# Optimization experiments

Hardware: AMD Instinct MI355X
Metric: run time of the kernel (lower is better)

The kernel has to match this reference:

```python
import jax, jax.numpy as jnp
import numpy as np

B, A, S, D = 32, 32, 128, 1024
N, H = 16, 64


def setup_inputs() -> dict:
    key = jax.random.key(0)
    k1, k2, k3, k4, k5, k6 = jax.random.split(key, 6)
    encoder_outputs = jax.random.normal(k1, (B, A, S, D), dtype=jnp.float32)
    doc_attention_mask = jax.random.randint(k2, (B, A), 0, 2, dtype=jnp.int32)
    # DenseEinsum params: kernel [D, N, H], bias [N, H] (glorot / zeros)
    scale = (6.0 / (D + N * H)) ** 0.5
    wq = jax.random.uniform(k3, (D, N, H), jnp.float32, -scale, scale)
    wk = jax.random.uniform(k4, (D, N, H), jnp.float32, -scale, scale)
    bq = jnp.zeros((N, H), jnp.float32)
    bk = jnp.zeros((N, H), jnp.float32)
    return {"encoder_outputs": encoder_outputs, "doc_attention_mask": doc_attention_mask,
            "wq": wq, "bq": bq, "wk": wk, "bk": bk}


def reference(encoder_outputs, doc_attention_mask, wq, bq, wk, bk):
    # CLS embedding per doc: [B, A, D]
    cls = encoder_outputs[:, :, 0, :]
    m = doc_attention_mask.astype(jnp.float32)  # [B, A]
    # projections -> [B, A, N, H], masked per doc
    query = (jnp.einsum('bad,dnh->banh', cls, wq) + bq) * m[:, :, None, None]
    key = (jnp.einsum('bad,dnh->banh', cls, wk) + bk) * m[:, :, None, None]
    # pairwise doc scores [B, N, A, A]
    att = jnp.einsum('bxnh,bynh->bnxy', query, key)
    num_docs = att.shape[-1]
    diag_mask = 1.0 - jnp.eye(num_docs, dtype=att.dtype)  # zero diagonal
    att = att * diag_mask
    # BNXY -> BNX (sum over Y) -> BX (sum over N)
    logits = att.sum(axis=(1, 3))  # [B, A]
    infadder = (1.0 - m) * -100000.0
    return jax.nn.softmax(logits + infadder, axis=-1)
```

## Files before the change

### kernel.cpp

```cpp
#include <hip/hip_runtime.h>
#include <hip/hip_bf16.h>


#define RB 1024
#define DD 1024
#define CC 1024
#define ENC_ROW_STRIDE (128 * 1024)

#define BM 64
#define BN 64
#define BK 32

__global__ __launch_bounds__(256) void gemm_qk_logits(
    const float* __restrict__ enc, const int* __restrict__ mask,
    const float* __restrict__ wq, const float* __restrict__ wk,
    const float* __restrict__ bq, const float* __restrict__ bk,
    float* __restrict__ logits)
{
    __shared__ __align__(16) float As[BK][BM + 4];
    __shared__ __align__(16) float Bqs[BK][BN];
    __shared__ __align__(16) float Bks[BK][BN];
    __shared__ float ksum_s[2][BN];

    const int tid  = threadIdx.x;
    const int row0 = blockIdx.y * BM;
    const int col0 = blockIdx.x * BN;

    const int tx = tid & 15;
    const int ty = tid >> 4;

    const int ar = tid >> 5, ac = tid & 31;
    const int br = tid >> 6, bc = tid & 63;

    float accq[4][4] = {{0.f}}, acck[4][4] = {{0.f}};

    for (int k0 = 0; k0 < DD; k0 += BK) {
        #pragma unroll
        for (int r = 0; r < 8; ++r) {
            int m = ar + 8 * r;
            As[ac][m] = enc[(size_t)(row0 + m) * ENC_ROW_STRIDE + k0 + ac];
        }
        #pragma unroll
        for (int r = 0; r < 8; ++r) {
            int kk = br + 4 * r;
            size_t off = (size_t)(k0 + kk) * CC + col0 + bc;
            Bqs[kk][bc] = wq[off];
            Bks[kk][bc] = wk[off];
        }
        __syncthreads();

        #pragma unroll
        for (int kk = 0; kk < BK; ++kk) {
            float4 a4 = *(const float4*)&As[kk][ty * 4];
            float4 q4 = *(const float4*)&Bqs[kk][tx * 4];
            float4 k4 = *(const float4*)&Bks[kk][tx * 4];
            float a[4]   = {a4.x, a4.y, a4.z, a4.w};
            float bqv[4] = {q4.x, q4.y, q4.z, q4.w};
            float bkv[4] = {k4.x, k4.y, k4.z, k4.w};
            #pragma unroll
            for (int i = 0; i < 4; ++i) {
                #pragma unroll
                for (int j = 0; j < 4; ++j) {
                    accq[i][j] = fmaf(a[i], bqv[j], accq[i][j]);
                    acck[i][j] = fmaf(a[i], bkv[j], acck[i][j]);
                }
            }
        }
        __syncthreads();
    }

    const int bat = ty >> 3;

    if (tid < 2 * BN) ((float*)ksum_s)[tid] = 0.f;
    __syncthreads();

    float qv[4][4], kv[4][4];
    float mrow[4];
    #pragma unroll
    for (int i = 0; i < 4; ++i) {
        int row = row0 + ty * 4 + i;
        mrow[i] = (float)mask[row];
    }
    #pragma unroll
    for (int j = 0; j < 4; ++j) {
        int col = col0 + tx * 4 + j;
        float bqc = bq[col], bkc = bk[col];
        float ks = 0.f;
        #pragma unroll
        for (int i = 0; i < 4; ++i) {
            qv[i][j] = (accq[i][j] + bqc) * mrow[i];
            kv[i][j] = (acck[i][j] + bkc) * mrow[i];
            ks += kv[i][j];
        }
        atomicAdd(&ksum_s[bat][tx * 4 + j], ks);
    }
    __syncthreads();

    #pragma unroll
    for (int i = 0; i < 4; ++i) {
        float p = 0.f;
        #pragma unroll
        for (int j = 0; j < 4; ++j)
            p = fmaf(qv[i][j], ksum_s[bat][tx * 4 + j] - kv[i][j], p);
        #pragma unroll
        for (int off = 8; off; off >>= 1) p += __shfl_down(p, off, 16);
        if (tx == 0) atomicAdd(&logits[row0 + ty * 4 + i], p);
    }
}

__global__ __launch_bounds__(1024) void softmax32(
    const float* __restrict__ logits, const int* __restrict__ mask,
    float* __restrict__ out)
{
    const int t = threadIdx.x;
    float m = (float)mask[t];
    float v = logits[t] + (1.f - m) * -100000.f;
    float mx = v;
    #pragma unroll
    for (int off = 16; off; off >>= 1) mx = fmaxf(mx, __shfl_xor(mx, off, 32));
    float e = expf(v - mx);
    float s = e;
    #pragma unroll
    for (int off = 16; off; off >>= 1) s += __shfl_xor(s, off, 32);
    out[t] = e / s;
}

extern "C" void kernel_launch(void* const* d_in, const int* in_sizes, int n_in,
                              void* d_out, int out_size, void* d_ws, size_t ws_size,
                              hipStream_t stream) {
    const float* enc  = (const float*)d_in[0];
    const int*   mask = (const int*)  d_in[1];
    const float* wq   = (const float*)d_in[2];
    const float* bq   = (const float*)d_in[3];
    const float* wk   = (const float*)d_in[4];
    const float* bk   = (const float*)d_in[5];
    float* out = (float*)d_out;

    float* logits = (float*)d_ws;
    hipMemsetAsync(logits, 0, RB * sizeof(float), stream);

    gemm_qk_logits<<<dim3(CC / BN, RB / BM), 256, 0, stream>>>(
        enc, mask, wq, wk, bq, bk, logits);
    softmax32<<<1, 1024, 0, stream>>>(logits, mask, out);
}
```

Measured before the change: 698.8 us.

## Replace FP32 SIMT GEMM with bf16 MFMA GEMM using prepped transposed weights

Adds a prep kernel that converts the CLS rows and transposed Wq/Wk to bf16. The main GEMM now uses 16x16x32 bf16 MFMA instructions with direct global-to-LDS loads into XOR-swizzled shared tiles. Per-column-block partial logits are written to a buffer and summed in the softmax kernel, which replaces the memset and global atomics. This trades fp32 precision for bf16 inputs and adds an extra pass that rewrites the weights on every call.

```diff
diff --git a/kernel.cpp b/kernel.cpp
--- a/kernel.cpp
+++ b/kernel.cpp
@@ -1,5 +1,6 @@
 #include <hip/hip_runtime.h>
 #include <hip/hip_bf16.h>
+#include <stdint.h>
 
 
 #define RB 1024
@@ -7,114 +8,216 @@
 #define CC 1024
 #define ENC_ROW_STRIDE (128 * 1024)
 
-#define BM 64
-#define BN 64
-#define BK 32
-
-__global__ __launch_bounds__(256) void gemm_qk_logits(
-    const float* __restrict__ enc, const int* __restrict__ mask,
+typedef __attribute__((ext_vector_type(8))) short short8;
+typedef __attribute__((ext_vector_type(4))) float float4v;
+
+__device__ __forceinline__ unsigned short f2bf(float f) {
+    union { float f; unsigned int u; } x; x.f = f;
+    unsigned int r = (x.u + 0x7fffu + ((x.u >> 16) & 1u)) >> 16;
+    return (unsigned short)r;
+}
+
+__device__ __forceinline__ void gld_lds16(const void* g, void* l) {
+    __builtin_amdgcn_global_load_lds(
+        (const __attribute__((address_space(1))) void*)(uintptr_t)g,
+        (__attribute__((address_space(3))) void*)(uintptr_t)l,
+        16, 0, 0);
+}
+
+__global__ __launch_bounds__(256) void prep(
+    const float* __restrict__ enc,
     const float* __restrict__ wq, const float* __restrict__ wk,
+    unsigned short* __restrict__ Abf,
+    unsigned short* __restrict__ WTq, unsigned short* __restrict__ WTk)
+{
+    __shared__ float Ts[64][65];
+    const int bid = blockIdx.x, t = threadIdx.x;
+
+    if (bid < 512) {
+        const float* W = (bid < 256) ? wq : wk;
+        unsigned short* WT = (bid < 256) ? WTq : WTk;
+        const int tile = bid & 255;
+        const int k0 = (tile >> 4) * 64, n0 = (tile & 15) * 64;
+        const int nn = t & 63, kk0 = t >> 6;
+        #pragma unroll
+        for (int r = 0; r < 16; ++r) {
+            int kk = kk0 + 4 * r;
+            Ts[kk][nn] = W[(size_t)(k0 + kk) * CC + n0 + nn];
+        }
+        __syncthreads();
+        const int kp = t & 31, nb = t >> 5;
+        #pragma unroll
+        for (int r = 0; r < 8; ++r) {
+            int n2 = nb + 8 * r;
+            unsigned int lo = f2bf(Ts[2 * kp][n2]);
+            unsigned int hi = f2bf(Ts[2 * kp + 1][n2]);
+            ((unsigned int*)WT)[(((size_t)(n0 + n2)) * DD + k0) / 2 + kp] =
+                lo | (hi << 16);
+        }
+    } else {
+        const int r0 = (bid - 512) * 16;
+        const int rr = t >> 4, f = t & 15;
+        const float* src = enc + (size_t)(r0 + rr) * ENC_ROW_STRIDE;
+        unsigned short* dst = Abf + (size_t)(r0 + rr) * DD;
+        #pragma unroll
+        for (int i = 0; i < 16; ++i) {
+            int c4 = (f + 16 * i) * 4;
+            float4 v = *(const float4*)(src + c4);
+            ushort4 o;
+            o.x = f2bf(v.x); o.y = f2bf(v.y); o.z = f2bf(v.z); o.w = f2bf(v.w);
+            *(ushort4*)(dst + c4) = o;
+        }
+    }
+}
+
+__global__ __launch_bounds__(256) void gemm_mfma(
+    const unsigned short* __restrict__ Abf,
+    const unsigned short* __restrict__ WTq,
+    const unsigned short* __restrict__ WTk,
+    const int* __restrict__ mask,
     const float* __restrict__ bq, const float* __restrict__ bk,
-    float* __restrict__ logits)
+    float* __restrict__ lpart)
 {
-    __shared__ __align__(16) float As[BK][BM + 4];
-    __shared__ __align__(16) float Bqs[BK][BN];
-    __shared__ __align__(16) float Bks[BK][BN];
-    __shared__ float ksum_s[2][BN];
-
-    const int tid  = threadIdx.x;
-    const int row0 = blockIdx.y * BM;
-    const int col0 = blockIdx.x * BN;
-
-    const int tx = tid & 15;
-    const int ty = tid >> 4;
-
-    const int ar = tid >> 5, ac = tid & 31;
-    const int br = tid >> 6, bc = tid & 63;
-
-    float accq[4][4] = {{0.f}}, acck[4][4] = {{0.f}};
-
-    for (int k0 = 0; k0 < DD; k0 += BK) {
-        #pragma unroll
-        for (int r = 0; r < 8; ++r) {
-            int m = ar + 8 * r;
-            As[ac][m] = enc[(size_t)(row0 + m) * ENC_ROW_STRIDE + k0 + ac];
-        }
-        #pragma unroll
-        for (int r = 0; r < 8; ++r) {
-            int kk = br + 4 * r;
-            size_t off = (size_t)(k0 + kk) * CC + col0 + bc;
-            Bqs[kk][bc] = wq[off];
-            Bks[kk][bc] = wk[off];
-        }
+    __shared__ __align__(16) unsigned char As[8192];
+    __shared__ __align__(16) unsigned char Bqs[8192];
+    __shared__ __align__(16) unsigned char Bks[8192];
+    __shared__ float bq_s[64], bk_s[64];
+    __shared__ int mask_s[64];
+    __shared__ float plog[2][64];
+
+    const int tid = threadIdx.x;
+    const int wave = tid >> 6, lane = tid & 63;
+    const int wr = wave >> 1, wc = wave & 1;
+    const int quad = lane >> 4, c = lane & 15;
+    const int bx = blockIdx.x, by = blockIdx.y;
+    const int row0 = by * 64, n0 = bx * 64;
+
+    if (tid < 64) {
+        bq_s[tid] = bq[n0 + tid];
+        bk_s[tid] = bk[n0 + tid];
+        mask_s[tid] = mask[row0 + tid];
+    }
+
+    float4v accq[2][2] = {}, acck[2][2] = {};
+
+    const int srow = (lane >> 3);
+    const int qsrc = (lane & 7) ^ srow;
+
+    const char* Ab = (const char*)Abf;
+    const char* Qb = (const char*)WTq;
+    const char* Kb = (const char*)WTk;
+
+    for (int kt = 0; kt < 16; ++kt) {
         __syncthreads();
-
-        #pragma unroll
-        for (int kk = 0; kk < BK; ++kk) {
-            float4 a4 = *(const float4*)&As[kk][ty * 4];
-            float4 q4 = *(const float4*)&Bqs[kk][tx * 4];
-            float4 k4 = *(const float4*)&Bks[kk][tx * 4];
-            float a[4]   = {a4.x, a4.y, a4.z, a4.w};
-            float bqv[4] = {q4.x, q4.y, q4.z, q4.w};
-            float bkv[4] = {k4.x, k4.y, k4.z, k4.w};
-            #pragma unroll
-            for (int i = 0; i < 4; ++i) {
+        const int kbyte = kt * 128 + qsrc * 16;
+        #pragma unroll
+        for (int i = 0; i < 2; ++i) {
+            int m = wave * 16 + i * 8 + srow;
+            char* dA = (char*)As  + wave * 2048 + i * 1024;
+            char* dQ = (char*)Bqs + wave * 2048 + i * 1024;
+            char* dK = (char*)Bks + wave * 2048 + i * 1024;
+            gld_lds16(Ab + (size_t)(row0 + m) * 2048 + kbyte, dA);
+            gld_lds16(Qb + (size_t)(n0  + m) * 2048 + kbyte, dQ);
+            gld_lds16(Kb + (size_t)(n0  + m) * 2048 + kbyte, dK);
+        }
+        __syncthreads();
+
+        #pragma unroll
+        for (int ks = 0; ks < 2; ++ks) {
+            const int og = ks * 4 + quad;
+            short8 a[2], fq[2], fk[2];
+            #pragma unroll
+            for (int mt = 0; mt < 2; ++mt) {
+                int m = wr * 32 + mt * 16 + c;
+                int q = og ^ (m & 7);
+                a[mt] = *(const short8*)(As + m * 128 + q * 16);
+            }
+            #pragma unroll
+            for (int nt = 0; nt < 2; ++nt) {
+                int n = wc * 32 + nt * 16 + c;
+                int q = og ^ (n & 7);
+                fq[nt] = *(const short8*)(Bqs + n * 128 + q * 16);
+                fk[nt] = *(const short8*)(Bks + n * 128 + q * 16);
+            }
+            #pragma unroll
+            for (int mt = 0; mt < 2; ++mt)
                 #pragma unroll
-                for (int j = 0; j < 4; ++j) {
-                    accq[i][j] = fmaf(a[i], bqv[j], accq[i][j]);
-                    acck[i][j] = fmaf(a[i], bkv[j], acck[i][j]);
+                for (int nt = 0; nt < 2; ++nt) {
+                    accq[mt][nt] = __builtin_amdgcn_mfma_f32_16x16x32_bf16(
+                        a[mt], fq[nt], accq[mt][nt], 0, 0, 0);
+                    acck[mt][nt] = __builtin_amdgcn_mfma_f32_16x16x32_bf16(
+                        a[mt], fk[nt], acck[mt][nt], 0, 0, 0);
                 }
+        }
+    }
+
+    float qv[2][2][4], kv[2][2][4];
+    float mrow[2][4];
+    #pragma unroll
+    for (int mt = 0; mt < 2; ++mt)
+        #pragma unroll
+        for (int r = 0; r < 4; ++r)
+            mrow[mt][r] = (float)mask_s[wr * 32 + mt * 16 + quad * 4 + r];
+
+    float ksm[2] = {0.f, 0.f};
+    #pragma unroll
+    for (int nt = 0; nt < 2; ++nt) {
+        int ncol = wc * 32 + nt * 16 + c;
+        float bqc = bq_s[ncol], bkc = bk_s[ncol];
+        #pragma unroll
+        for (int mt = 0; mt < 2; ++mt)
+            #pragma unroll
+            for (int r = 0; r < 4; ++r) {
+                float mm = mrow[mt][r];
+                qv[mt][nt][r] = (accq[mt][nt][r] + bqc) * mm;
+                float kk = (acck[mt][nt][r] + bkc) * mm;
+                kv[mt][nt][r] = kk;
+                ksm[nt] += kk;
             }
-        }
-        __syncthreads();
-    }
-
-    const int bat = ty >> 3;
-
-    if (tid < 2 * BN) ((float*)ksum_s)[tid] = 0.f;
+    }
+    #pragma unroll
+    for (int nt = 0; nt < 2; ++nt) {
+        ksm[nt] += __shfl_xor(ksm[nt], 16, 64);
+        ksm[nt] += __shfl_xor(ksm[nt], 32, 64);
+    }
+
+    float pl[2][4];
+    #pragma unroll
+    for (int mt = 0; mt < 2; ++mt)
+        #pragma unroll
+        for (int r = 0; r < 4; ++r) {
+            float p = 0.f;
+            #pragma unroll
+            for (int nt = 0; nt < 2; ++nt)
+                p = fmaf(qv[mt][nt][r], ksm[nt] - kv[mt][nt][r], p);
+            p += __shfl_xor(p, 1, 64);
+            p += __shfl_xor(p, 2, 64);
+            p += __shfl_xor(p, 4, 64);
+            p += __shfl_xor(p, 8, 64);
+            pl[mt][r] = p;
+        }
+    if (c == 0) {
+        #pragma unroll
+        for (int mt = 0; mt < 2; ++mt)
+            #pragma unroll
+            for (int r = 0; r < 4; ++r)
+                plog[wc][wr * 32 + mt * 16 + quad * 4 + r] = pl[mt][r];
+    }
     __syncthreads();
-
-    float qv[4][4], kv[4][4];
-    float mrow[4];
-    #pragma unroll
-    for (int i = 0; i < 4; ++i) {
-        int row = row0 + ty * 4 + i;
-        mrow[i] = (float)mask[row];
-    }
-    #pragma unroll
-    for (int j = 0; j < 4; ++j) {
-        int col = col0 + tx * 4 + j;
-        float bqc = bq[col], bkc = bk[col];
-        float ks = 0.f;
-        #pragma unroll
-        for (int i = 0; i < 4; ++i) {
-            qv[i][j] = (accq[i][j] + bqc) * mrow[i];
-            kv[i][j] = (acck[i][j] + bkc) * mrow[i];
-            ks += kv[i][j];
-        }
-        atomicAdd(&ksum_s[bat][tx * 4 + j], ks);
-    }
-    __syncthreads();
-
-    #pragma unroll
-    for (int i = 0; i < 4; ++i) {
-        float p = 0.f;
-        #pragma unroll
-        for (int j = 0; j < 4; ++j)
-            p = fmaf(qv[i][j], ksum_s[bat][tx * 4 + j] - kv[i][j], p);
-        #pragma unroll
-        for (int off = 8; off; off >>= 1) p += __shfl_down(p, off, 16);
-        if (tx == 0) atomicAdd(&logits[row0 + ty * 4 + i], p);
-    }
-}
-
-__global__ __launch_bounds__(1024) void softmax32(
-    const float* __restrict__ logits, const int* __restrict__ mask,
+    if (tid < 64)
+        lpart[(size_t)bx * RB + row0 + tid] = plog[0][tid] + plog[1][tid];
+}
+
+__global__ __launch_bounds__(1024) void softmax_final(
+    const float* __restrict__ lpart, const int* __restrict__ mask,
     float* __restrict__ out)
 {
     const int t = threadIdx.x;
+    float lg = 0.f;
+    #pragma unroll
+    for (int c2 = 0; c2 < 16; ++c2) lg += lpart[c2 * RB + t];
     float m = (float)mask[t];
-    float v = logits[t] + (1.f - m) * -100000.f;
+    float v = lg + (1.f - m) * -100000.f;
     float mx = v;
     #pragma unroll
     for (int off = 16; off; off >>= 1) mx = fmaxf(mx, __shfl_xor(mx, off, 32));
@@ -136,10 +239,12 @@
     const float* bk   = (const float*)d_in[5];
     float* out = (float*)d_out;
 
-    float* logits = (float*)d_ws;
-    hipMemsetAsync(logits, 0, RB * sizeof(float), stream);
-
-    gemm_qk_logits<<<dim3(CC / BN, RB / BM), 256, 0, stream>>>(
-        enc, mask, wq, wk, bq, bk, logits);
-    softmax32<<<1, 1024, 0, stream>>>(logits, mask, out);
-}
+    unsigned short* Abf = (unsigned short*)d_ws;
+    unsigned short* WTq = Abf + (size_t)RB * DD;
+    unsigned short* WTk = WTq + (size_t)DD * CC;
+    float* lpart = (float*)(WTk + (size_t)DD * CC);
+
+    prep<<<576, 256, 0, stream>>>(enc, wq, wk, Abf, WTq, WTk);
+    gemm_mfma<<<dim3(16, 16), 256, 0, stream>>>(Abf, WTq, WTk, mask, bq, bk, lpart);
+    softmax_final<<<1, 1024, 0, stream>>>(lpart, mask, out);
+}
```

After: 594.5 us. 1.18x faster.
